# Kernel tuning notes

Measured on AMD Instinct MI355X. Metric: run time of the kernel, lower is better.

The kernel has to match this reference:

```python
import jax, jax.numpy as jnp
import numpy as np

STRIDE = 1
PAD_INIT = 0


def _im2col(x, k, stride, padding):
    # torch.nn.functional.unfold equivalent: channel order (C, kh, kw), row-major spatial
    patches = jax.lax.conv_general_dilated_patches(
        x, (k, k), (stride, stride), [(padding, padding), (padding, padding)])
    # patches: (N, C*k*k, h_out, w_out)
    N, d, ho, wo = patches.shape
    # match torch code: view(N, d, L').permute(1,2,0).reshape(d, L'*N)
    X_col = patches.reshape(N, d, ho * wo).transpose(1, 2, 0).reshape(d, ho * wo * N)
    return X_col, ho, wo


def setup_inputs() -> dict:
    key = jax.random.key(0)
    k1, k2 = jax.random.split(key)
    x = jax.random.normal(k1, (32, 128, 28, 28), dtype=jnp.float32)
    W = jax.random.normal(k2, (128, 128, 3, 3), dtype=jnp.float32)
    return {"x": x, "W": W}


def reference(x, W):
    F_, C, kh, kw = W.shape
    N, _, H, _ = x.shape
    # 'full' conv output size per the module's formula
    h_out = (H - 1) * STRIDE - 2 * PAD_INIT + (kh - 1) + 1
    pad = ((h_out - 1) * STRIDE + kh - H) // 2
    X_col, ho, wo = _im2col(x, kh, STRIDE, pad)          # (d, L), d=C*k*k, L=ho*wo*N
    W_col = W.reshape(F_, -1)                            # (F, d)
    # intended quadratic 'adder' decomposition: out[f,l] = -0.5*||W_f - X_l||^2
    # = W_f . X_l - 0.5*||W_f||^2 - 0.5*||X_l||^2  (fused GEMM form, no (F,d,L) blowup)
    out = (W_col @ X_col
           - 0.5 * jnp.sum(W_col * W_col, axis=1)[:, None]
           - 0.5 * jnp.sum(X_col * X_col, axis=0)[None, :])  # (F, L)
    out = out.reshape(F_, ho, wo, N).transpose(3, 0, 1, 2)   # (N, F, ho, wo)
    return out
```

## Files before the change

kernel.cpp:

```cpp
#include <hip/hip_runtime.h>
#include <hip/hip_bf16.h>
#include <stdint.h>


#define N_IMG 32
#define C_IN 128
#define H_IN 28
#define HP 32
#define HO 30
#define P_SP 900
#define F_OUT 128
#define K_TOT 1152

#define BLT 60
#define TPI 15
#define NBLK (N_IMG*TPI)
#define NSTEP 18

typedef __attribute__((ext_vector_type(8))) short bf16x8;
typedef __attribute__((ext_vector_type(4))) unsigned short u16x4;
typedef __attribute__((ext_vector_type(8))) unsigned short u16x8;
typedef __attribute__((ext_vector_type(4))) float f32x4;

__device__ __forceinline__ unsigned short f2bf(float f) {
  union { float f; unsigned u; } t; t.f = f;
  unsigned r = t.u + 0x7fffu + ((t.u >> 16) & 1u);
  return (unsigned short)(r >> 16);
}

__global__ void prep_w_kernel(const float* __restrict__ W,
                              unsigned short* __restrict__ Wbf,
                              float* __restrict__ wnorm) {
  int f = blockIdx.x;
  const float* Wf = W + f * K_TOT;
  float part = 0.f;
  for (int k = threadIdx.x; k < K_TOT; k += 256) {
    float v = Wf[k];
    part += v * v;
    int ch = k / 9, rr = k - ch * 9;
    Wbf[f * K_TOT + rr * 128 + ch] = f2bf(v);
  }
  __shared__ float red[256];
  red[threadIdx.x] = part;
  __syncthreads();
  for (int st = 128; st > 0; st >>= 1) {
    if (threadIdx.x < st) red[threadIdx.x] += red[threadIdx.x + st];
    __syncthreads();
  }
  if (threadIdx.x == 0) wnorm[f] = 0.5f * red[0];
}

__global__ __launch_bounds__(512, 4) void adder_fused_kernel(
    const float* __restrict__ x,
    const unsigned short* __restrict__ Wbf,
    const float* __restrict__ wnorm,
    float* __restrict__ out) {
  __shared__ unsigned short xfoot[128 * 130];
  __shared__ unsigned short A_lds[2][64 * 128];
  __shared__ float pixsum_s[128];
  __shared__ float xn_s[64];
  __shared__ float wn_s[F_OUT];

  int tid = threadIdx.x, lane = tid & 63, wid = tid >> 6;
  int bid0 = blockIdx.x;
  int bid = (bid0 & 7) * (NBLK / 8) + (bid0 >> 3);
  int n = bid / TPI, timg = bid - n * TPI;
  int i0 = timg * 2, p0 = timg * BLT;

  char* XF = (char*)xfoot;
  char* A0 = (char*)&A_lds[0][0];
  char* A1 = (char*)&A_lds[1][0];
  const char* WbfB = (const char*)Wbf;

  int kb = ((lane & 7) * 16) ^ ((lane >> 3) << 4);
  int a_goff[2];
#pragma unroll
  for (int a = 0; a < 2; a++) {
    int q = a * 8 + wid;
    int rowf = q * 8 + (lane >> 3);
    a_goff[a] = rowf * (K_TOT * 2) + kb;
  }
  int a_loff = wid * 1024 + lane * 16;

  auto STAGE = [&](int t, char* AB) {
    int off = t * 128;
#pragma unroll
    for (int a = 0; a < 2; a++)
      __builtin_amdgcn_global_load_lds(
          (const __attribute__((address_space(1))) void*)(WbfB + a_goff[a] + off),
          (__attribute__((address_space(3))) void*)(AB + a * 8192 + a_loff), 16, 0, 0);
  };

  if (tid < F_OUT) wn_s[tid] = wnorm[tid];
  STAGE(0, A0);
  STAGE(1, A1);

  for (int u = tid; u < 896; u += 512) {
    int cq = u / 28, rem = u - cq * 28;
    int r = rem / 7, w4 = rem - r * 7;
    int c = cq * 4;
    int hr = i0 - 2 + r;
    float vv[4][4];
    if (hr >= 0 && hr < H_IN) {
#pragma unroll
      for (int q = 0; q < 4; q++) {
        float4 t4 = *(const float4*)(x + (((n * C_IN + c + q) * H_IN + hr) * H_IN + w4 * 4));
        vv[q][0] = t4.x; vv[q][1] = t4.y; vv[q][2] = t4.z; vv[q][3] = t4.w;
      }
    } else {
#pragma unroll
      for (int q = 0; q < 4; q++)
#pragma unroll
        for (int e = 0; e < 4; e++) vv[q][e] = 0.f;
    }
#pragma unroll
    for (int e = 0; e < 4; e++) {
      int wp = w4 * 4 + e + 2;
      int pix = r * 32 + wp;
      u16x4 o;
#pragma unroll
      for (int q = 0; q < 4; q++) o[q] = f2bf(vv[q][e]);
      *(u16x4*)(XF + pix * 256 + ((c * 2) ^ ((pix & 15) << 4))) = o;
    }
  }
  if (tid < 256) {
    int r = tid >> 6, wi = (tid >> 4) & 3, slot = tid & 15;
    int wp = (wi < 2) ? wi : 28 + wi;
    int pix = r * 32 + wp;
    u16x8 z;
#pragma unroll
    for (int q = 0; q < 8; q++) z[q] = 0;
    *(u16x8*)(XF + pix * 256 + ((slot * 16) ^ ((pix & 15) << 4))) = z;
  }
  __syncthreads();

  if (tid < 256) {
    int pix = tid >> 1, ch = tid & 1;
    float ssum = 0.f;
#pragma unroll
    for (int q = 0; q < 8; q++) {
      u16x8 v8 = *(const u16x8*)(XF + pix * 256 + (((ch * 128) + q * 16) ^ ((pix & 15) << 4)));
#pragma unroll
      for (int e = 0; e < 8; e++) {
        union { unsigned u; float f; } cv; cv.u = ((unsigned)v8[e]) << 16;
        ssum += cv.f * cv.f;
      }
    }
    ssum += __shfl_xor(ssum, 1);
    if (!ch) pixsum_s[pix] = ssum;
  }
  __syncthreads();
  if (tid < BLT) {
    int il = tid / HO, j = tid - il * HO;
    float a9 = 0.f;
#pragma unroll
    for (int dh = 0; dh < 3; dh++)
#pragma unroll
      for (int dw = 0; dw < 3; dw++)
        a9 += pixsum_s[(il + dh) * 32 + (j + dw)];
    xn_s[tid] = 0.5f * a9;
  }
  __syncthreads();

  f32x4 acc[2][2];
#pragma unroll
  for (int mi = 0; mi < 2; mi++)
#pragma unroll
    for (int ni = 0; ni < 2; ni++)
      acc[mi][ni] = (f32x4){0.f, 0.f, 0.f, 0.f};

  int wr = wid >> 1, wc = wid & 1;
  int colc = lane & 15, kg = lane >> 4;
  int kfrag = kg * 16;
  int pix0[2];
#pragma unroll
  for (int ni = 0; ni < 2; ni++) {
    int cc = wc * 32 + ni * 16 + colc;
    if (cc > BLT - 1) cc = BLT - 1;
    int il = cc / HO, j = cc - il * HO;
    pix0[ni] = il * 32 + j;
  }
  int arow[2], asw[2];
#pragma unroll
  for (int mi = 0; mi < 2; mi++) {
    int rowf = wr * 32 + mi * 16 + colc;
    arow[mi] = rowf * 128;
    asw[mi] = (rowf & 7) << 4;
  }

#pragma unroll 2
  for (int t = 0; t < NSTEP; t++) {
    char* ABc = (t & 1) ? A1 : A0;
    int rr = t >> 1, half = t & 1;
    int dh = rr / 3, dw = rr - 3 * dh;
    int pofs = dh * 32 + dw;
    int bbase = half * 128;
#pragma unroll
    for (int kc = 0; kc < 2; kc++) {
      bf16x8 af[2], bfv[2];
#pragma unroll
      for (int mi = 0; mi < 2; mi++)
        af[mi] = *(const bf16x8*)(ABc + arow[mi] + ((kc * 64 + kfrag) ^ asw[mi]));
#pragma unroll
      for (int ni = 0; ni < 2; ni++) {
        int pix = pix0[ni] + pofs;
        bfv[ni] = *(const bf16x8*)(XF + pix * 256 + ((bbase + kc * 64 + kfrag) ^ ((pix & 15) << 4)));
      }
      __builtin_amdgcn_s_setprio(1);
#pragma unroll
      for (int mi = 0; mi < 2; mi++)
#pragma unroll
        for (int ni = 0; ni < 2; ni++)
          acc[mi][ni] = __builtin_amdgcn_mfma_f32_16x16x32_bf16(
              af[mi], bfv[ni], acc[mi][ni], 0, 0, 0);
      __builtin_amdgcn_s_setprio(0);
    }
    __builtin_amdgcn_s_barrier();
    if (t + 2 < NSTEP) {
      STAGE(t + 2, ABc);
      asm volatile("s_waitcnt vmcnt(2)" ::: "memory");
      __builtin_amdgcn_s_barrier();
    } else if (t + 2 == NSTEP) {
      asm volatile("s_waitcnt vmcnt(0)" ::: "memory");
      __builtin_amdgcn_s_barrier();
    }
  }
  __syncthreads();

  float* Cst = (float*)xfoot;
#pragma unroll
  for (int mi = 0; mi < 2; mi++) {
    int f0 = wr * 32 + mi * 16 + kg * 4;
#pragma unroll
    for (int ni = 0; ni < 2; ni++) {
      int cc = wc * 32 + ni * 16 + colc;
#pragma unroll
      for (int r = 0; r < 4; r++)
        Cst[(f0 + r) * 65 + cc] = acc[mi][ni][r];
    }
  }
  __syncthreads();
  {
    int col = tid & 63, fq = tid >> 6;
    if (col < BLT) {
      float xn = xn_s[col];
      float* ob = out + (size_t)n * (F_OUT * P_SP) + p0 + col;
#pragma unroll
      for (int q = 0; q < 16; q++) {
        int f = fq * 16 + q;
        __builtin_nontemporal_store(Cst[f * 65 + col] - wn_s[f] - xn, ob + f * P_SP);
      }
    }
  }
}

extern "C" void kernel_launch(void* const* d_in, const int* in_sizes, int n_in,
                              void* d_out, int out_size, void* d_ws, size_t ws_size,
                              hipStream_t stream) {
  const float* x = (const float*)d_in[0];
  const float* W = (const float*)d_in[1];
  float* out = (float*)d_out;

  char* ws = (char*)d_ws;
  unsigned short* Wbf = (unsigned short*)(ws);
  float* wnorm = (float*)(ws + 294912);

  prep_w_kernel<<<F_OUT, 256, 0, stream>>>(W, Wbf, wnorm);
  adder_fused_kernel<<<NBLK, 512, 0, stream>>>(x, Wbf, wnorm, out);
}
```

Baseline: 26.03 us.

## Store weights and input footprint in k-chunk-major fragment layout for MFMA

Weights are pre-permuted into 8-element k-chunk-major blocks, so each staging step copies one contiguous 16 KB slab straight into LDS. The input footprint in LDS moves from a swizzled pixel-major layout to a channel-chunk-major one. Operand addresses become a base pointer plus a compile-time immediate, and the main loop is fully unrolled. This removes per-iteration XOR and address arithmetic, but the new LDS layout may cause bank conflicts and full unrolling increases code size.

New measurement: 24.80 us (median of 2 runs). 1.05x faster.

```diff
diff --git a/kernel.cpp b/kernel.cpp
--- a/kernel.cpp
+++ b/kernel.cpp
@@ -29,7 +29,7 @@
 }
 
 __global__ void prep_w_kernel(const float* __restrict__ W,
-                              unsigned short* __restrict__ Wbf,
+                              unsigned short* __restrict__ Wfrag2,
                               float* __restrict__ wnorm) {
   int f = blockIdx.x;
   const float* Wf = W + f * K_TOT;
@@ -38,7 +38,8 @@
     float v = Wf[k];
     part += v * v;
     int ch = k / 9, rr = k - ch * 9;
-    Wbf[f * K_TOT + rr * 128 + ch] = f2bf(v);
+    int kp = rr * 128 + ch;
+    Wfrag2[(kp >> 3) * 1024 + f * 8 + (kp & 7)] = f2bf(v);
   }
   __shared__ float red[256];
   red[threadIdx.x] = part;
@@ -52,7 +53,7 @@
 
 __global__ __launch_bounds__(512, 4) void adder_fused_kernel(
     const float* __restrict__ x,
-    const unsigned short* __restrict__ Wbf,
+    const unsigned short* __restrict__ Wfrag2,
     const float* __restrict__ wnorm,
     float* __restrict__ out) {
   __shared__ unsigned short xfoot[128 * 130];
@@ -70,25 +71,19 @@
   char* XF = (char*)xfoot;
   char* A0 = (char*)&A_lds[0][0];
   char* A1 = (char*)&A_lds[1][0];
-  const char* WbfB = (const char*)Wbf;
-
-  int kb = ((lane & 7) * 16) ^ ((lane >> 3) << 4);
-  int a_goff[2];
-#pragma unroll
-  for (int a = 0; a < 2; a++) {
-    int q = a * 8 + wid;
-    int rowf = q * 8 + (lane >> 3);
-    a_goff[a] = rowf * (K_TOT * 2) + kb;
-  }
-  int a_loff = wid * 1024 + lane * 16;
+  const char* WfB = (const char*)Wfrag2;
+
+  int a_off[2];
+#pragma unroll
+  for (int a = 0; a < 2; a++) a_off[a] = (a * 8 + wid) * 1024 + lane * 16;
 
   auto STAGE = [&](int t, char* AB) {
-    int off = t * 128;
+    const char* src = WfB + t * 16384;
 #pragma unroll
     for (int a = 0; a < 2; a++)
       __builtin_amdgcn_global_load_lds(
-          (const __attribute__((address_space(1))) void*)(WbfB + a_goff[a] + off),
-          (__attribute__((address_space(3))) void*)(AB + a * 8192 + a_loff), 16, 0, 0);
+          (const __attribute__((address_space(1))) void*)(src + a_off[a]),
+          (__attribute__((address_space(3))) void*)(AB + a_off[a]), 16, 0, 0);
   };
 
   if (tid < F_OUT) wn_s[tid] = wnorm[tid];
@@ -120,7 +115,7 @@
       u16x4 o;
 #pragma unroll
       for (int q = 0; q < 4; q++) o[q] = f2bf(vv[q][e]);
-      *(u16x4*)(XF + pix * 256 + ((c * 2) ^ ((pix & 15) << 4))) = o;
+      *(u16x4*)(XF + (c >> 3) * 2048 + pix * 16 + (c & 4) * 2) = o;
     }
   }
   if (tid < 256) {
@@ -130,7 +125,7 @@
     u16x8 z;
 #pragma unroll
     for (int q = 0; q < 8; q++) z[q] = 0;
-    *(u16x8*)(XF + pix * 256 + ((slot * 16) ^ ((pix & 15) << 4))) = z;
+    *(u16x8*)(XF + slot * 2048 + pix * 16) = z;
   }
   __syncthreads();
 
@@ -139,7 +134,7 @@
     float ssum = 0.f;
 #pragma unroll
     for (int q = 0; q < 8; q++) {
-      u16x8 v8 = *(const u16x8*)(XF + pix * 256 + (((ch * 128) + q * 16) ^ ((pix & 15) << 4)));
+      u16x8 v8 = *(const u16x8*)(XF + (ch * 8 + q) * 2048 + pix * 16);
 #pragma unroll
       for (int e = 0; e < 8; e++) {
         union { unsigned u; float f; } cv; cv.u = ((unsigned)v8[e]) << 16;
@@ -171,41 +166,38 @@
 
   int wr = wid >> 1, wc = wid & 1;
   int colc = lane & 15, kg = lane >> 4;
-  int kfrag = kg * 16;
-  int pix0[2];
+
+  const char* Ab[2][2];
+#pragma unroll
+  for (int mi = 0; mi < 2; mi++) {
+    int rowf = wr * 32 + mi * 16 + colc;
+    Ab[0][mi] = A0 + kg * 2048 + rowf * 16;
+    Ab[1][mi] = A1 + kg * 2048 + rowf * 16;
+  }
+  const char* Bb[2];
 #pragma unroll
   for (int ni = 0; ni < 2; ni++) {
     int cc = wc * 32 + ni * 16 + colc;
     if (cc > BLT - 1) cc = BLT - 1;
     int il = cc / HO, j = cc - il * HO;
-    pix0[ni] = il * 32 + j;
-  }
-  int arow[2], asw[2];
-#pragma unroll
-  for (int mi = 0; mi < 2; mi++) {
-    int rowf = wr * 32 + mi * 16 + colc;
-    arow[mi] = rowf * 128;
-    asw[mi] = (rowf & 7) << 4;
-  }
-
-#pragma unroll 2
+    Bb[ni] = XF + kg * 2048 + (il * 32 + j) * 16;
+  }
+
+#pragma unroll
   for (int t = 0; t < NSTEP; t++) {
-    char* ABc = (t & 1) ? A1 : A0;
-    int rr = t >> 1, half = t & 1;
-    int dh = rr / 3, dw = rr - 3 * dh;
-    int pofs = dh * 32 + dw;
-    int bbase = half * 128;
+    const int buf = t & 1;
+    const int rr = t >> 1, half = t & 1;
+    const int dh = rr / 3, dw = rr - 3 * dh;
+    const int bimm = half * 16384 + (dh * 32 + dw) * 16;
 #pragma unroll
     for (int kc = 0; kc < 2; kc++) {
       bf16x8 af[2], bfv[2];
 #pragma unroll
       for (int mi = 0; mi < 2; mi++)
-        af[mi] = *(const bf16x8*)(ABc + arow[mi] + ((kc * 64 + kfrag) ^ asw[mi]));
-#pragma unroll
-      for (int ni = 0; ni < 2; ni++) {
-        int pix = pix0[ni] + pofs;
-        bfv[ni] = *(const bf16x8*)(XF + pix * 256 + ((bbase + kc * 64 + kfrag) ^ ((pix & 15) << 4)));
-      }
+        af[mi] = *(const bf16x8*)(Ab[buf][mi] + kc * 8192);
+#pragma unroll
+      for (int ni = 0; ni < 2; ni++)
+        bfv[ni] = *(const bf16x8*)(Bb[ni] + bimm + kc * 8192);
       __builtin_amdgcn_s_setprio(1);
 #pragma unroll
       for (int mi = 0; mi < 2; mi++)
@@ -217,7 +209,7 @@
     }
     __builtin_amdgcn_s_barrier();
     if (t + 2 < NSTEP) {
-      STAGE(t + 2, ABc);
+      STAGE(t + 2, buf ? A1 : A0);
       asm volatile("s_waitcnt vmcnt(2)" ::: "memory");
       __builtin_amdgcn_s_barrier();
     } else if (t + 2 == NSTEP) {
@@ -228,9 +220,10 @@
   __syncthreads();
 
   float* Cst = (float*)xfoot;
+  int kg4 = kg * 4;
 #pragma unroll
   for (int mi = 0; mi < 2; mi++) {
-    int f0 = wr * 32 + mi * 16 + kg * 4;
+    int f0 = wr * 32 + mi * 16 + kg4;
 #pragma unroll
     for (int ni = 0; ni < 2; ni++) {
       int cc = wc * 32 + ni * 16 + colc;
@@ -262,9 +255,9 @@
   float* out = (float*)d_out;
 
   char* ws = (char*)d_ws;
-  unsigned short* Wbf = (unsigned short*)(ws);
+  unsigned short* Wfrag2 = (unsigned short*)(ws);
   float* wnorm = (float*)(ws + 294912);
 
-  prep_w_kernel<<<F_OUT, 256, 0, stream>>>(W, Wbf, wnorm);
-  adder_fused_kernel<<<NBLK, 512, 0, stream>>>(x, Wbf, wnorm, out);
-}
+  prep_w_kernel<<<F_OUT, 256, 0, stream>>>(W, Wfrag2, wnorm);
+  adder_fused_kernel<<<NBLK, 512, 0, stream>>>(x, Wfrag2, wnorm, out);
+}
```
